# Performance work log

Measured on AMD Instinct MI355X. Metric: run time of the kernel, lower is better.

Reference implementation:

```python
import jax, jax.numpy as jnp
import numpy as np


def setup_inputs() -> dict:
    key = jax.random.key(0)
    ks = jax.random.split(key, 4)
    B, S, D, U = 4, 4096, 128, 64
    x = jax.random.normal(ks[0], (B, S, D), dtype=jnp.float32)
    Wq = jax.random.normal(ks[1], (D, U), dtype=jnp.float32) * (1.0 / np.sqrt(D))
    Wk = jax.random.normal(ks[2], (D, U), dtype=jnp.float32) * (1.0 / np.sqrt(D))
    Wv = jax.random.normal(ks[3], (D, U), dtype=jnp.float32) * (1.0 / np.sqrt(D))
    bq = jnp.zeros((U,), dtype=jnp.float32)
    bk = jnp.zeros((U,), dtype=jnp.float32)
    bv = jnp.zeros((U,), dtype=jnp.float32)
    return {"x": x, "Wq": Wq, "bq": bq, "Wk": Wk, "bk": bk, "Wv": Wv, "bv": bv}


def reference(x, Wq, bq, Wk, bk, Wv, bv):
    # Single-head, unscaled, unmasked attention (faithful to the Keras layer).
    q = jnp.einsum("bsd,du->bsu", x, Wq) + bq  # [B,S,U]
    k = jnp.einsum("bsd,du->bsu", x, Wk) + bk  # [B,S,U]
    v = jnp.einsum("bsd,du->bsu", x, Wv) + bv  # [B,S,U]
    scores = jnp.einsum("bsu,btu->bst", q, k)  # [B,S,S], no 1/sqrt(d) scaling
    attn = jax.nn.softmax(scores, axis=-1)
    return jnp.einsum("bst,btu->bsu", attn, v)  # [B,S,U]
```

## Files before the change

### kernel.cpp

```cpp
#include <hip/hip_runtime.h>
#include <hip/hip_fp16.h>
#include <math.h>

#define SEQ   4096
#define DIM   128
#define UDIM  64
#define BATCH 4
#define BS    (BATCH*SEQ)
#define NT    (SEQ/64)
#define NSPLIT 6

typedef _Float16 h8 __attribute__((ext_vector_type(8)));
typedef _Float16 h4 __attribute__((ext_vector_type(4)));
typedef _Float16 h2 __attribute__((ext_vector_type(2)));
typedef float    f4 __attribute__((ext_vector_type(4)));

#define MFMA_K32(a,b,c) __builtin_amdgcn_mfma_f32_16x16x32_f16((a),(b),(c),0,0,0)

__device__ __forceinline__ h2 pk2(float a, float b) {
  return __builtin_bit_cast(h2, __builtin_amdgcn_cvt_pkrtz(a, b));
}
__device__ __forceinline__ float fexp2(float x) {
#if __has_builtin(__builtin_amdgcn_exp2f)
  return __builtin_amdgcn_exp2f(x);
#else
  return exp2f(x);
#endif
}

#define WT_STRIDE 272
#define KB_STRIDE 144
#define L2E 1.44269504088896f


__global__ __launch_bounds__(256, 2) void proj_mfma(
    const float* __restrict__ x,
    const float* __restrict__ Wq, const float* __restrict__ bq,
    const float* __restrict__ Wk, const float* __restrict__ bk,
    const float* __restrict__ Wv, const float* __restrict__ bv,
    _Float16* __restrict__ qf, _Float16* __restrict__ kswz, _Float16* __restrict__ vswz)
{
  const int tid  = threadIdx.x;
  const int lane = tid & 63, wv = tid >> 6;
  const int n = lane & 15, quad = lane >> 4;
  const int r0 = blockIdx.x * 64;

  __shared__ __align__(16) char wlds[3][UDIM * WT_STRIDE];
  __shared__ __align__(16) char kbnc[4 * 16 * KB_STRIDE];

  #pragma unroll
  for (int p = 0; p < 3; ++p) {
    const float* __restrict__ W = (p == 0) ? Wq : ((p == 1) ? Wk : Wv);
    #pragma unroll
    for (int i = 0; i < 8; ++i) {
      const int idx = i*256 + tid;
      const int nn  = idx & 63;
      const int k4  = (idx >> 6) * 4;
      const float w0 = W[(k4+0)*UDIM + nn];
      const float w1 = W[(k4+1)*UDIM + nn];
      const float w2 = W[(k4+2)*UDIM + nn];
      const float w3 = W[(k4+3)*UDIM + nn];
      int2 wd;
      wd.x = __builtin_bit_cast(int, pk2(w0, w1));
      wd.y = __builtin_bit_cast(int, pk2(w2, w3));
      *(int2*)(wlds[p] + nn*WT_STRIDE + k4*2) = wd;
    }
  }

  const int row = r0 + wv*16 + n;
  h8 xa[4];
  #pragma unroll
  for (int ks = 0; ks < 4; ++ks) {
    const float* xp = x + (size_t)row*DIM + ks*32 + quad*8;
    const f4 a = *(const f4*)xp, b = *(const f4*)(xp + 4);
    int4 pkd;
    pkd.x = __builtin_bit_cast(int, pk2(a[0], a[1]));
    pkd.y = __builtin_bit_cast(int, pk2(a[2], a[3]));
    pkd.z = __builtin_bit_cast(int, pk2(b[0], b[1]));
    pkd.w = __builtin_bit_cast(int, pk2(b[2], b[3]));
    xa[ks] = __builtin_bit_cast(h8, pkd);
  }
  __syncthreads();

  const int b  = r0 / SEQ;
  const int kb = ((r0 % SEQ) >> 4) + wv;
  const int vt = (r0 % SEQ) >> 6;

  #pragma unroll
  for (int p = 0; p < 3; ++p) {
    const float* __restrict__ bias = (p == 0) ? bq : ((p == 1) ? bk : bv);
    f4 acc[4];
    #pragma unroll
    for (int nt = 0; nt < 4; ++nt) acc[nt] = (f4){0.f,0.f,0.f,0.f};
    #pragma unroll
    for (int ks = 0; ks < 4; ++ks)
      #pragma unroll
      for (int nt = 0; nt < 4; ++nt) {
        const h8 wf = *(const h8*)(wlds[p] + (nt*16 + n)*WT_STRIDE + (ks*32 + quad*8)*2);
        acc[nt] = MFMA_K32(xa[ks], wf, acc[nt]);
      }
    #pragma unroll
    for (int nt = 0; nt < 4; ++nt) {
      const float bb = bias[nt*16 + n];
      #pragma unroll
      for (int r = 0; r < 4; ++r) acc[nt][r] += bb;
    }

    if (p == 0) {
      #pragma unroll
      for (int nt = 0; nt < 4; ++nt)
        #pragma unroll
        for (int r = 0; r < 4; ++r) acc[nt][r] *= L2E;
      const int par = lane & 1;
      const unsigned sel = par ? 0x03020706u : 0x05040100u;
      #pragma unroll
      for (int nt = 0; nt < 4; ++nt)
        #pragma unroll
        for (int pp = 0; pp < 2; ++pp) {
          const int r = 2*pp;
          unsigned A  = __builtin_bit_cast(unsigned, pk2(acc[nt][r], acc[nt][r+1]));
          unsigned Bs = (unsigned)__builtin_amdgcn_mov_dpp((int)A, 0xB1, 0xF, 0xF, true);
          unsigned w  = __builtin_amdgcn_perm(Bs, A, sel);
          const int orow = r0 + wv*16 + 4*quad + r + par;
          const int ocol = nt*16 + n - par;
          *(unsigned*)((char*)qf + ((size_t)orow*UDIM + ocol)*2) = w;
        }
    } else if (p == 1) {
      char* base = kbnc + wv*(16*KB_STRIDE);
      #pragma unroll
      for (int nt = 0; nt < 4; ++nt)
        #pragma unroll
        for (int r = 0; r < 4; ++r)
          *(_Float16*)(base + (4*quad + r)*KB_STRIDE + (nt*16 + n)*2) =
              (_Float16)acc[nt][r];
      _Float16* kdst = kswz + (size_t)b*SEQ*UDIM;
      #pragma unroll
      for (int ks = 0; ks < 2; ++ks) {
        const h8 f = *(const h8*)(base + n*KB_STRIDE + ks*64 + quad*16);
        *(h8*)(kdst + ((size_t)(kb*2 + ks)*64 + lane)*8) = f;
      }
    } else {
      _Float16* vdst = vswz + (size_t)b*SEQ*UDIM + (size_t)vt*4096;
      const int hh = wv >> 1;
      const int qp = 2*(wv & 1) + (quad >> 1);
      const int jb = (quad & 1) * 4;
      #pragma unroll
      for (int nt = 0; nt < 4; ++nt) {
        int2 t;
        t.x = __builtin_bit_cast(int, pk2(acc[nt][0], acc[nt][1]));
        t.y = __builtin_bit_cast(int, pk2(acc[nt][2], acc[nt][3]));
        *(int2*)(vdst + (hh*4 + nt)*512 + (16*qp + n)*8 + jb) = t;
      }
    }
  }
}

__global__ __launch_bounds__(256, 3) void flash_attn_t(
    const _Float16* __restrict__ qf, const _Float16* __restrict__ kswz,
    const _Float16* __restrict__ vswz,
    _Float16* __restrict__ opart, float* __restrict__ Mp, float* __restrict__ Lp)
{
  const int qt = blockIdx.x, b = blockIdx.y, sp = blockIdx.z;
  const int ns = gridDim.z;
  const int kt0 = (sp * NT) / ns;
  const int kt1 = ((sp + 1) * NT) / ns;
  const int tid = threadIdx.x;
  const int lane = tid & 63, wid = tid >> 6;
  const int n = lane & 15, quad = lane >> 4;
  const int qbase = qt*128 + wid*32;

  const _Float16* __restrict__ qb = qf + (size_t)b*SEQ*UDIM;
  const _Float16* kpl = kswz + (size_t)b*SEQ*UDIM + (size_t)kt0*4096 + lane*8;
  const _Float16* kph = kpl + 2048;
  const _Float16* vpl = vswz + (size_t)b*SEQ*UDIM + (size_t)kt0*4096 + lane*8;
  const _Float16* vph = vpl + 2048;

  h8 qB[2][2];
  #pragma unroll
  for (int nt = 0; nt < 2; ++nt)
    #pragma unroll
    for (int ks = 0; ks < 2; ++ks)
      qB[nt][ks] = *(const h8*)(qb + (size_t)(qbase + nt*16 + n)*UDIM + ks*32 + quad*8);

  f4 O[4][2], Ol[2];
  #pragma unroll
  for (int ut = 0; ut < 4; ++ut)
    #pragma unroll
    for (int nt = 0; nt < 2; ++nt) O[ut][nt] = (f4){0.f,0.f,0.f,0.f};
  Ol[0] = (f4){0.f,0.f,0.f,0.f};
  Ol[1] = (f4){0.f,0.f,0.f,0.f};

  float M[2] = {-1e30f, -1e30f};

  h8 ones8;
  { const _Float16 o = (_Float16)1.0f;
    #pragma unroll
    for (int i = 0; i < 8; ++i) ones8[i] = o; }

  const int alo4 = ((32*((lane >> 4) & 1) + (lane & 15)) << 2);
  const int ahi4 = alo4 + 64;
  const bool qlo = (lane < 32);

  h8 ka[4][2];
  ka[0][0] = *(const h8*)(kpl);        ka[0][1] = *(const h8*)(kpl +  512);
  ka[1][0] = *(const h8*)(kpl + 1024); ka[1][1] = *(const h8*)(kpl + 1536);
  ka[2][0] = *(const h8*)(kph);        ka[2][1] = *(const h8*)(kph +  512);
  ka[3][0] = *(const h8*)(kph + 1024); ka[3][1] = *(const h8*)(kph + 1536);

  for (int t = kt0; t < kt1; ++t) {
    h8 va0[4];
    va0[0] = *(const h8*)(vpl);        va0[1] = *(const h8*)(vpl +  512);
    va0[2] = *(const h8*)(vpl + 1024); va0[3] = *(const h8*)(vpl + 1536);

    f4 S[4][2];
    #pragma unroll
    for (int mt = 0; mt < 4; ++mt)
      #pragma unroll
      for (int nt = 0; nt < 2; ++nt) S[mt][nt] = (f4){0.f,0.f,0.f,0.f};
    #pragma unroll
    for (int ks = 0; ks < 2; ++ks)
      #pragma unroll
      for (int mt = 0; mt < 4; ++mt)
        #pragma unroll
        for (int nt = 0; nt < 2; ++nt)
          S[mt][nt] = MFMA_K32(ka[mt][ks], qB[nt][ks], S[mt][nt]);

    if (t + 1 < kt1) {
      kpl += 4096; kph += 4096;
      ka[0][0] = *(const h8*)(kpl);        ka[0][1] = *(const h8*)(kpl +  512);
      ka[1][0] = *(const h8*)(kpl + 1024); ka[1][1] = *(const h8*)(kpl + 1536);
      ka[2][0] = *(const h8*)(kph);        ka[2][1] = *(const h8*)(kph +  512);
      ka[3][0] = *(const h8*)(kph + 1024); ka[3][1] = *(const h8*)(kph + 1536);
    }

    float mn[2];
    #pragma unroll
    for (int nt = 0; nt < 2; ++nt) {
      float m0 = fmaxf(fmaxf(S[0][nt][0], S[0][nt][1]), fmaxf(S[0][nt][2], S[0][nt][3]));
      float m1 = fmaxf(fmaxf(S[1][nt][0], S[1][nt][1]), fmaxf(S[1][nt][2], S[1][nt][3]));
      float m2 = fmaxf(fmaxf(S[2][nt][0], S[2][nt][1]), fmaxf(S[2][nt][2], S[2][nt][3]));
      float m3 = fmaxf(fmaxf(S[3][nt][0], S[3][nt][1]), fmaxf(S[3][nt][2], S[3][nt][3]));
      float rm = fmaxf(fmaxf(m0, m1), fmaxf(m2, m3));
      rm = fmaxf(rm, __shfl_xor(rm, 16));
      rm = fmaxf(rm, __shfl_xor(rm, 32));
      mn[nt] = fmaxf(M[nt], rm);
    }

    const bool nochange = (mn[0] == M[0]) && (mn[1] == M[1]);
    if (!__all(nochange)) {
      #pragma unroll
      for (int nt = 0; nt < 2; ++nt) {
        const float alpha = fexp2(M[nt] - mn[nt]);
        #pragma unroll
        for (int ut = 0; ut < 4; ++ut)
          #pragma unroll
          for (int r = 0; r < 4; ++r) O[ut][nt][r] *= alpha;
        #pragma unroll
        for (int r = 0; r < 4; ++r) Ol[nt][r] *= alpha;
      }
    }
    M[0] = mn[0]; M[1] = mn[1];

    h4 pB[4][2];
    #pragma unroll
    for (int mt = 0; mt < 4; ++mt)
      #pragma unroll
      for (int nt = 0; nt < 2; ++nt) {
        #pragma unroll
        for (int r = 0; r < 4; ++r)
          S[mt][nt][r] = fexp2(S[mt][nt][r] - mn[nt]);
        int2 tt;
        tt.x = __builtin_bit_cast(int, pk2(S[mt][nt][0], S[mt][nt][1]));
        tt.y = __builtin_bit_cast(int, pk2(S[mt][nt][2], S[mt][nt][3]));
        pB[mt][nt] = __builtin_bit_cast(h4, tt);
      }

    h8 pb32a[2];
    #pragma unroll
    for (int nt = 0; nt < 2; ++nt) {
      const int2 X = __builtin_bit_cast(int2, pB[0][nt]);
      const int2 Y = __builtin_bit_cast(int2, pB[1][nt]);
      int4 o;
      { int a0 = __builtin_amdgcn_ds_bpermute(alo4, X.x);
        int b0 = __builtin_amdgcn_ds_bpermute(alo4, Y.x);
        int a1 = __builtin_amdgcn_ds_bpermute(alo4, X.y);
        int b1 = __builtin_amdgcn_ds_bpermute(alo4, Y.y);
        int a2 = __builtin_amdgcn_ds_bpermute(ahi4, X.x);
        int b2 = __builtin_amdgcn_ds_bpermute(ahi4, Y.x);
        int a3 = __builtin_amdgcn_ds_bpermute(ahi4, X.y);
        int b3 = __builtin_amdgcn_ds_bpermute(ahi4, Y.y);
        o.x = qlo ? a0 : b0; o.y = qlo ? a1 : b1;
        o.z = qlo ? a2 : b2; o.w = qlo ? a3 : b3; }
      pb32a[nt] = __builtin_bit_cast(h8, o);
    }

    h8 va1[4];
    va1[0] = *(const h8*)(vph);        va1[1] = *(const h8*)(vph +  512);
    va1[2] = *(const h8*)(vph + 1024); va1[3] = *(const h8*)(vph + 1536);

    #pragma unroll
    for (int ut = 0; ut < 4; ++ut)
      #pragma unroll
      for (int nt = 0; nt < 2; ++nt)
        O[ut][nt] = MFMA_K32(va0[ut], pb32a[nt], O[ut][nt]);
    #pragma unroll
    for (int nt = 0; nt < 2; ++nt)
      Ol[nt] = MFMA_K32(ones8, pb32a[nt], Ol[nt]);

    h8 pb32b[2];
    #pragma unroll
    for (int nt = 0; nt < 2; ++nt) {
      const int2 X = __builtin_bit_cast(int2, pB[2][nt]);
      const int2 Y = __builtin_bit_cast(int2, pB[3][nt]);
      int4 o;
      { int a0 = __builtin_amdgcn_ds_bpermute(alo4, X.x);
        int b0 = __builtin_amdgcn_ds_bpermute(alo4, Y.x);
        int a1 = __builtin_amdgcn_ds_bpermute(alo4, X.y);
        int b1 = __builtin_amdgcn_ds_bpermute(alo4, Y.y);
        int a2 = __builtin_amdgcn_ds_bpermute(ahi4, X.x);
        int b2 = __builtin_amdgcn_ds_bpermute(ahi4, Y.x);
        int a3 = __builtin_amdgcn_ds_bpermute(ahi4, X.y);
        int b3 = __builtin_amdgcn_ds_bpermute(ahi4, Y.y);
        o.x = qlo ? a0 : b0; o.y = qlo ? a1 : b1;
        o.z = qlo ? a2 : b2; o.w = qlo ? a3 : b3; }
      pb32b[nt] = __builtin_bit_cast(h8, o);
    }

    #pragma unroll
    for (int ut = 0; ut < 4; ++ut)
      #pragma unroll
      for (int nt = 0; nt < 2; ++nt)
        O[ut][nt] = MFMA_K32(va1[ut], pb32b[nt], O[ut][nt]);
    #pragma unroll
    for (int nt = 0; nt < 2; ++nt)
      Ol[nt] = MFMA_K32(ones8, pb32b[nt], Ol[nt]);

    vpl += 4096; vph += 4096;
  }

  const size_t rowg = (size_t)sp*BS + (size_t)b*SEQ + qbase;
  #pragma unroll
  for (int nt = 0; nt < 2; ++nt) {
    char* __restrict__ orow = (char*)(opart + (rowg + nt*16 + n)*UDIM);
    #pragma unroll
    for (int ut = 0; ut < 4; ++ut)
      #pragma unroll
      for (int p = 0; p < 2; ++p)
        *(unsigned*)(orow + (ut*16 + quad*4 + 2*p)*2) =
            __builtin_bit_cast(unsigned, pk2(O[ut][nt][2*p], O[ut][nt][2*p+1]));
    if (quad == 0) {
      Mp[rowg + nt*16 + n] = M[nt];
      Lp[rowg + nt*16 + n] = Ol[nt][0];
    }
  }
}

__global__ __launch_bounds__(256) void merge_out(
    const _Float16* __restrict__ opart, const float* __restrict__ Mp,
    const float* __restrict__ Lp, float* __restrict__ out, int nsplit)
{
  const int tid = threadIdx.x;
  const int row = blockIdx.x*16 + (tid >> 4);
  const int u4  = (tid & 15) * 4;
  float M = -1e30f;
  for (int s = 0; s < nsplit; ++s) M = fmaxf(M, Mp[(size_t)s*BS + row]);
  f4 num = (f4){0.f,0.f,0.f,0.f};
  float den = 0.f;
  for (int s = 0; s < nsplit; ++s) {
    const float w = fexp2(Mp[(size_t)s*BS + row] - M);
    den += w * Lp[(size_t)s*BS + row];
    const h4 op = *(const h4*)(opart + ((size_t)s*BS + row)*UDIM + u4);
    #pragma unroll
    for (int i = 0; i < 4; ++i) num[i] += w * (float)op[i];
  }
  const float dinv = 1.f / den;
  *(f4*)(out + (size_t)row*UDIM + u4) = num * dinv;
}

extern "C" void kernel_launch(void* const* d_in, const int* in_sizes, int n_in,
                              void* d_out, int out_size, void* d_ws, size_t ws_size,
                              hipStream_t stream) {
  (void)in_sizes; (void)n_in; (void)out_size;
  const float* x  = (const float*)d_in[0];
  const float* Wq = (const float*)d_in[1];
  const float* bq = (const float*)d_in[2];
  const float* Wk = (const float*)d_in[3];
  const float* bk = (const float*)d_in[4];
  const float* Wv = (const float*)d_in[5];
  const float* bv = (const float*)d_in[6];
  float* out = (float*)d_out;

  char* ws = (char*)d_ws;
  const size_t fBytes = (size_t)BS * UDIM * 2;
  auto need = [](int nsp) {
    return (size_t)3*BS*UDIM*2 + (size_t)nsp*BS*4*2 + (size_t)nsp*BS*UDIM*2;
  };
  int nsplit;
  if      (ws_size >= need(NSPLIT)) nsplit = NSPLIT;
  else if (ws_size >= need(4))      nsplit = 4;
  else if (ws_size >= need(2))      nsplit = 2;
  else                              nsplit = 1;

  _Float16* qf   = (_Float16*)(ws);
  _Float16* kswz = (_Float16*)(ws + fBytes);
  _Float16* vswz = (_Float16*)(ws + 2*fBytes);
  float* Mp      = (float*)(ws + 3*fBytes);
  float* Lp      = (float*)(ws + 3*fBytes + (size_t)nsplit*BS*4);
  _Float16* opart = (_Float16*)(ws + 3*fBytes + (size_t)nsplit*BS*8);

  proj_mfma<<<dim3(BS/64), 256, 0, stream>>>(x, Wq, bq, Wk, bk, Wv, bv, qf, kswz, vswz);
  flash_attn_t<<<dim3(SEQ/128, BATCH, nsplit), 256, 0, stream>>>(
      qf, kswz, vswz, opart, Mp, Lp);
  merge_out<<<dim3(BS/16), 256, 0, stream>>>(opart, Mp, Lp, out, nsplit);
}
```

Before: 109.6 us.

## Stage K/V tiles into double-buffered LDS via global_load_lds shared across waves

Replaces per-wave direct global loads of K and V tiles with a block-wide asynchronous global-to-LDS copy into a double buffer. Each wave stages one quarter of the next tile, then all waves read K and V fragments from LDS. Before, each of the four waves fetched the full tile from global/L2 itself, so this cuts that redundant traffic and overlaps the fetch with compute. In exchange it adds 32KB of LDS per block, which may limit occupancy, plus a barrier per iteration and LDS read latency. It also relies on the barrier to ensure the async copies have completed.

```diff
diff --git a/kernel.cpp b/kernel.cpp
--- a/kernel.cpp
+++ b/kernel.cpp
@@ -26,6 +26,12 @@
 #else
   return exp2f(x);
 #endif
+}
+
+__device__ __forceinline__ void stage16(const void* g, void* l) {
+  __builtin_amdgcn_global_load_lds(
+      (const __attribute__((address_space(1))) unsigned int*)g,
+      (__attribute__((address_space(3))) unsigned int*)l, 16, 0, 0);
 }
 
 #define WT_STRIDE 272
@@ -169,12 +175,24 @@
   const int n = lane & 15, quad = lane >> 4;
   const int qbase = qt*128 + wid*32;
 
+  __shared__ __align__(16) char kv[2][16384];
+
+  const char* __restrict__ kbase = (const char*)kswz + (size_t)b*SEQ*UDIM*2;
+  const char* __restrict__ vbase = (const char*)vswz + (size_t)b*SEQ*UDIM*2;
+  const int s0 = wid*2;
+  const int lb = lane*16;
+
+  {
+    const char* kb_ = kbase + (size_t)kt0*8192;
+    const char* vb_ = vbase + (size_t)kt0*8192;
+    #pragma unroll
+    for (int s = 0; s < 2; ++s) {
+      stage16(kb_ + (s0+s)*1024 + lb, &kv[0][(s0+s)*1024]);
+      stage16(vb_ + (s0+s)*1024 + lb, &kv[0][8192 + (s0+s)*1024]);
+    }
+  }
+
   const _Float16* __restrict__ qb = qf + (size_t)b*SEQ*UDIM;
-  const _Float16* kpl = kswz + (size_t)b*SEQ*UDIM + (size_t)kt0*4096 + lane*8;
-  const _Float16* kph = kpl + 2048;
-  const _Float16* vpl = vswz + (size_t)b*SEQ*UDIM + (size_t)kt0*4096 + lane*8;
-  const _Float16* vph = vpl + 2048;
-
   h8 qB[2][2];
   #pragma unroll
   for (int nt = 0; nt < 2; ++nt)
@@ -201,16 +219,30 @@
   const int ahi4 = alo4 + 64;
   const bool qlo = (lane < 32);
 
-  h8 ka[4][2];
-  ka[0][0] = *(const h8*)(kpl);        ka[0][1] = *(const h8*)(kpl +  512);
-  ka[1][0] = *(const h8*)(kpl + 1024); ka[1][1] = *(const h8*)(kpl + 1536);
-  ka[2][0] = *(const h8*)(kph);        ka[2][1] = *(const h8*)(kph +  512);
-  ka[3][0] = *(const h8*)(kph + 1024); ka[3][1] = *(const h8*)(kph + 1536);
-
+  __syncthreads();
+
+  int cur = 0;
   for (int t = kt0; t < kt1; ++t) {
-    h8 va0[4];
-    va0[0] = *(const h8*)(vpl);        va0[1] = *(const h8*)(vpl +  512);
-    va0[2] = *(const h8*)(vpl + 1024); va0[3] = *(const h8*)(vpl + 1536);
+    if (t + 1 < kt1) {
+      const char* kb_ = kbase + (size_t)(t+1)*8192;
+      const char* vb_ = vbase + (size_t)(t+1)*8192;
+      char* dst = kv[cur ^ 1];
+      #pragma unroll
+      for (int s = 0; s < 2; ++s) {
+        stage16(kb_ + (s0+s)*1024 + lb, dst + (s0+s)*1024);
+        stage16(vb_ + (s0+s)*1024 + lb, dst + 8192 + (s0+s)*1024);
+      }
+    }
+
+    const char* Kl = kv[cur] + lb;
+    const char* Vl = Kl + 8192;
+
+    h8 ka[4][2];
+    #pragma unroll
+    for (int mt = 0; mt < 4; ++mt)
+      #pragma unroll
+      for (int ks = 0; ks < 2; ++ks)
+        ka[mt][ks] = *(const h8*)(Kl + (mt*2 + ks)*1024);
 
     f4 S[4][2];
     #pragma unroll
@@ -224,14 +256,6 @@
         #pragma unroll
         for (int nt = 0; nt < 2; ++nt)
           S[mt][nt] = MFMA_K32(ka[mt][ks], qB[nt][ks], S[mt][nt]);
-
-    if (t + 1 < kt1) {
-      kpl += 4096; kph += 4096;
-      ka[0][0] = *(const h8*)(kpl);        ka[0][1] = *(const h8*)(kpl +  512);
-      ka[1][0] = *(const h8*)(kpl + 1024); ka[1][1] = *(const h8*)(kpl + 1536);
-      ka[2][0] = *(const h8*)(kph);        ka[2][1] = *(const h8*)(kph +  512);
-      ka[3][0] = *(const h8*)(kph + 1024); ka[3][1] = *(const h8*)(kph + 1536);
-    }
 
     float mn[2];
     #pragma unroll
@@ -294,9 +318,9 @@
       pb32a[nt] = __builtin_bit_cast(h8, o);
     }
 
-    h8 va1[4];
-    va1[0] = *(const h8*)(vph);        va1[1] = *(const h8*)(vph +  512);
-    va1[2] = *(const h8*)(vph + 1024); va1[3] = *(const h8*)(vph + 1536);
+    h8 va0[4];
+    #pragma unroll
+    for (int ut = 0; ut < 4; ++ut) va0[ut] = *(const h8*)(Vl + ut*1024);
 
     #pragma unroll
     for (int ut = 0; ut < 4; ++ut)
@@ -326,6 +350,10 @@
       pb32b[nt] = __builtin_bit_cast(h8, o);
     }
 
+    h8 va1[4];
+    #pragma unroll
+    for (int ut = 0; ut < 4; ++ut) va1[ut] = *(const h8*)(Vl + (4 + ut)*1024);
+
     #pragma unroll
     for (int ut = 0; ut < 4; ++ut)
       #pragma unroll
@@ -335,7 +363,8 @@
     for (int nt = 0; nt < 2; ++nt)
       Ol[nt] = MFMA_K32(ones8, pb32b[nt], Ol[nt]);
 
-    vpl += 4096; vph += 4096;
+    if (t + 1 < kt1) __syncthreads();
+    cur ^= 1;
   }
 
   const size_t rowg = (size_t)sp*BS + (size_t)b*SEQ + qbase;
```

Result: slower. 114.0 us (+4.0%).

## Fuse projection, attention and merge into one cooperative kernel with grid syncs

Applied to the files above, without the earlier changes.

Merges the three launches (QKV projection, split-K flash attention, merge) into a single cooperative kernel of 256 blocks × 512 threads, separated by grid-wide syncs. The split count drops from 6 to 4 so that the 256 blocks × 8 waves map exactly onto the attention work items. This removes launch overhead and inter-kernel gaps. In exchange it adds grid barriers and gives less parallelism in the attention phase, with 2048 waves on 256 CUs. The workspace-size fallback is removed.

```diff
diff --git a/kernel.cpp b/kernel.cpp
--- a/kernel.cpp
+++ b/kernel.cpp
@@ -1,6 +1,9 @@
 #include <hip/hip_runtime.h>
 #include <hip/hip_fp16.h>
+#include <hip/hip_cooperative_groups.h>
 #include <math.h>
+
+namespace cg = cooperative_groups;
 
 #define SEQ   4096
 #define DIM   128
@@ -8,7 +11,7 @@
 #define BATCH 4
 #define BS    (BATCH*SEQ)
 #define NT    (SEQ/64)
-#define NSPLIT 6
+#define NSPLIT 4
 
 typedef _Float16 h8 __attribute__((ext_vector_type(8)));
 typedef _Float16 h4 __attribute__((ext_vector_type(4)));
@@ -33,116 +36,131 @@
 #define L2E 1.44269504088896f
 
 
-__global__ __launch_bounds__(256, 2) void proj_mfma(
+__global__ __launch_bounds__(512, 2) void fused_attn(
     const float* __restrict__ x,
     const float* __restrict__ Wq, const float* __restrict__ bq,
     const float* __restrict__ Wk, const float* __restrict__ bk,
     const float* __restrict__ Wv, const float* __restrict__ bv,
-    _Float16* __restrict__ qf, _Float16* __restrict__ kswz, _Float16* __restrict__ vswz)
+    _Float16* __restrict__ qf, _Float16* __restrict__ kswz,
+    _Float16* __restrict__ vswz,
+    _Float16* __restrict__ opart, float* __restrict__ Mp,
+    float* __restrict__ Lp, float* __restrict__ out)
 {
+  cg::grid_group grid = cg::this_grid();
   const int tid  = threadIdx.x;
-  const int lane = tid & 63, wv = tid >> 6;
+  const int lane = tid & 63, wid = tid >> 6;
   const int n = lane & 15, quad = lane >> 4;
-  const int r0 = blockIdx.x * 64;
 
   __shared__ __align__(16) char wlds[3][UDIM * WT_STRIDE];
   __shared__ __align__(16) char kbnc[4 * 16 * KB_STRIDE];
 
-  #pragma unroll
-  for (int p = 0; p < 3; ++p) {
-    const float* __restrict__ W = (p == 0) ? Wq : ((p == 1) ? Wk : Wv);
-    #pragma unroll
-    for (int i = 0; i < 8; ++i) {
-      const int idx = i*256 + tid;
-      const int nn  = idx & 63;
-      const int k4  = (idx >> 6) * 4;
-      const float w0 = W[(k4+0)*UDIM + nn];
-      const float w1 = W[(k4+1)*UDIM + nn];
-      const float w2 = W[(k4+2)*UDIM + nn];
-      const float w3 = W[(k4+3)*UDIM + nn];
-      int2 wd;
-      wd.x = __builtin_bit_cast(int, pk2(w0, w1));
-      wd.y = __builtin_bit_cast(int, pk2(w2, w3));
-      *(int2*)(wlds[p] + nn*WT_STRIDE + k4*2) = wd;
-    }
-  }
-
-  const int row = r0 + wv*16 + n;
-  h8 xa[4];
-  #pragma unroll
-  for (int ks = 0; ks < 4; ++ks) {
-    const float* xp = x + (size_t)row*DIM + ks*32 + quad*8;
-    const f4 a = *(const f4*)xp, b = *(const f4*)(xp + 4);
-    int4 pkd;
-    pkd.x = __builtin_bit_cast(int, pk2(a[0], a[1]));
-    pkd.y = __builtin_bit_cast(int, pk2(a[2], a[3]));
-    pkd.z = __builtin_bit_cast(int, pk2(b[0], b[1]));
-    pkd.w = __builtin_bit_cast(int, pk2(b[2], b[3]));
-    xa[ks] = __builtin_bit_cast(h8, pkd);
-  }
-  __syncthreads();
-
-  const int b  = r0 / SEQ;
-  const int kb = ((r0 % SEQ) >> 4) + wv;
-  const int vt = (r0 % SEQ) >> 6;
-
-  #pragma unroll
-  for (int p = 0; p < 3; ++p) {
-    const float* __restrict__ bias = (p == 0) ? bq : ((p == 1) ? bk : bv);
-    f4 acc[4];
-    #pragma unroll
-    for (int nt = 0; nt < 4; ++nt) acc[nt] = (f4){0.f,0.f,0.f,0.f};
-    #pragma unroll
-    for (int ks = 0; ks < 4; ++ks)
+  {
+    const int r0 = blockIdx.x * 64;
+
+    #pragma unroll
+    for (int p = 0; p < 3; ++p) {
+      const float* __restrict__ W = (p == 0) ? Wq : ((p == 1) ? Wk : Wv);
+      #pragma unroll
+      for (int i = 0; i < 4; ++i) {
+        const int idx = i*512 + tid;
+        const int nn  = idx & 63;
+        const int k4  = (idx >> 6) * 4;
+        const float w0 = W[(k4+0)*UDIM + nn];
+        const float w1 = W[(k4+1)*UDIM + nn];
+        const float w2 = W[(k4+2)*UDIM + nn];
+        const float w3 = W[(k4+3)*UDIM + nn];
+        int2 wd;
+        wd.x = __builtin_bit_cast(int, pk2(w0, w1));
+        wd.y = __builtin_bit_cast(int, pk2(w2, w3));
+        *(int2*)(wlds[p] + nn*WT_STRIDE + k4*2) = wd;
+      }
+    }
+
+    const int g    = wid & 3;
+    const int half = wid >> 2;
+    const int row  = r0 + g*16 + n;
+    h8 xa[4];
+    #pragma unroll
+    for (int ks = 0; ks < 4; ++ks) {
+      const float* xp = x + (size_t)row*DIM + ks*32 + quad*8;
+      const f4 a = *(const f4*)xp, bb2 = *(const f4*)(xp + 4);
+      int4 pkd;
+      pkd.x = __builtin_bit_cast(int, pk2(a[0], a[1]));
+      pkd.y = __builtin_bit_cast(int, pk2(a[2], a[3]));
+      pkd.z = __builtin_bit_cast(int, pk2(bb2[0], bb2[1]));
+      pkd.w = __builtin_bit_cast(int, pk2(bb2[2], bb2[3]));
+      xa[ks] = __builtin_bit_cast(h8, pkd);
+    }
+    __syncthreads();
+
+    const int b  = r0 / SEQ;
+    const int kb = ((r0 % SEQ) >> 4) + g;
+    const int vt = (r0 % SEQ) >> 6;
+
+    auto gemm16 = [&](const char* wp, const float* bias, f4* acc) {
+      #pragma unroll
+      for (int nt = 0; nt < 4; ++nt) acc[nt] = (f4){0.f,0.f,0.f,0.f};
+      #pragma unroll
+      for (int ks = 0; ks < 4; ++ks)
+        #pragma unroll
+        for (int nt = 0; nt < 4; ++nt) {
+          const h8 wf = *(const h8*)(wp + (nt*16 + n)*WT_STRIDE + (ks*32 + quad*8)*2);
+          acc[nt] = MFMA_K32(xa[ks], wf, acc[nt]);
+        }
       #pragma unroll
       for (int nt = 0; nt < 4; ++nt) {
-        const h8 wf = *(const h8*)(wlds[p] + (nt*16 + n)*WT_STRIDE + (ks*32 + quad*8)*2);
-        acc[nt] = MFMA_K32(xa[ks], wf, acc[nt]);
-      }
-    #pragma unroll
-    for (int nt = 0; nt < 4; ++nt) {
-      const float bb = bias[nt*16 + n];
-      #pragma unroll
-      for (int r = 0; r < 4; ++r) acc[nt][r] += bb;
-    }
-
-    if (p == 0) {
-      #pragma unroll
-      for (int nt = 0; nt < 4; ++nt)
-        #pragma unroll
-        for (int r = 0; r < 4; ++r) acc[nt][r] *= L2E;
-      const int par = lane & 1;
-      const unsigned sel = par ? 0x03020706u : 0x05040100u;
-      #pragma unroll
-      for (int nt = 0; nt < 4; ++nt)
-        #pragma unroll
-        for (int pp = 0; pp < 2; ++pp) {
-          const int r = 2*pp;
-          unsigned A  = __builtin_bit_cast(unsigned, pk2(acc[nt][r], acc[nt][r+1]));
-          unsigned Bs = (unsigned)__builtin_amdgcn_mov_dpp((int)A, 0xB1, 0xF, 0xF, true);
-          unsigned w  = __builtin_amdgcn_perm(Bs, A, sel);
-          const int orow = r0 + wv*16 + 4*quad + r + par;
-          const int ocol = nt*16 + n - par;
-          *(unsigned*)((char*)qf + ((size_t)orow*UDIM + ocol)*2) = w;
+        const float bb = bias[nt*16 + n];
+        #pragma unroll
+        for (int r = 0; r < 4; ++r) acc[nt][r] += bb;
+      }
+    };
+
+    if (half == 0) {
+      {
+        f4 acc[4];
+        gemm16(wlds[0], bq, acc);
+        #pragma unroll
+        for (int nt = 0; nt < 4; ++nt)
+          #pragma unroll
+          for (int r = 0; r < 4; ++r) acc[nt][r] *= L2E;
+        const int par = lane & 1;
+        const unsigned sel = par ? 0x03020706u : 0x05040100u;
+        #pragma unroll
+        for (int nt = 0; nt < 4; ++nt)
+          #pragma unroll
+          for (int pp = 0; pp < 2; ++pp) {
+            const int r = 2*pp;
+            unsigned A  = __builtin_bit_cast(unsigned, pk2(acc[nt][r], acc[nt][r+1]));
+            unsigned Bs = (unsigned)__builtin_amdgcn_mov_dpp((int)A, 0xB1, 0xF, 0xF, true);
+            unsigned w  = __builtin_amdgcn_perm(Bs, A, sel);
+            const int orow = r0 + g*16 + 4*quad + r + par;
+            const int ocol = nt*16 + n - par;
+            *(unsigned*)((char*)qf + ((size_t)orow*UDIM + ocol)*2) = w;
+          }
+      }
+      {
+        f4 acc[4];
+        gemm16(wlds[1], bk, acc);
+        char* base = kbnc + g*(16*KB_STRIDE);
+        #pragma unroll
+        for (int nt = 0; nt < 4; ++nt)
+          #pragma unroll
+          for (int r = 0; r < 4; ++r)
+            *(_Float16*)(base + (4*quad + r)*KB_STRIDE + (nt*16 + n)*2) =
+                (_Float16)acc[nt][r];
+        _Float16* kdst = kswz + (size_t)b*SEQ*UDIM;
+        #pragma unroll
+        for (int ks = 0; ks < 2; ++ks) {
+          const h8 f = *(const h8*)(base + n*KB_STRIDE + ks*64 + quad*16);
+          *(h8*)(kdst + ((size_t)(kb*2 + ks)*64 + lane)*8) = f;
         }
-    } else if (p == 1) {
-      char* base = kbnc + wv*(16*KB_STRIDE);
-      #pragma unroll
-      for (int nt = 0; nt < 4; ++nt)
-        #pragma unroll
-        for (int r = 0; r < 4; ++r)
-          *(_Float16*)(base + (4*quad + r)*KB_STRIDE + (nt*16 + n)*2) =
-              (_Float16)acc[nt][r];
-      _Float16* kdst = kswz + (size_t)b*SEQ*UDIM;
-      #pragma unroll
-      for (int ks = 0; ks < 2; ++ks) {
-        const h8 f = *(const h8*)(base + n*KB_STRIDE + ks*64 + quad*16);
-        *(h8*)(kdst + ((size_t)(kb*2 + ks)*64 + lane)*8) = f;
       }
     } else {
+      f4 acc[4];
+      gemm16(wlds[2], bv, acc);
       _Float16* vdst = vswz + (size_t)b*SEQ*UDIM + (size_t)vt*4096;
-      const int hh = wv >> 1;
-      const int qp = 2*(wv & 1) + (quad >> 1);
+      const int hh = g >> 1;
+      const int qp = 2*(g & 1) + (quad >> 1);
       const int jb = (quad & 1) * 4;
       #pragma unroll
       for (int nt = 0; nt < 4; ++nt) {
@@ -153,234 +171,238 @@
       }
     }
   }
-}
-
-__global__ __launch_bounds__(256, 3) void flash_attn_t(
-    const _Float16* __restrict__ qf, const _Float16* __restrict__ kswz,
-    const _Float16* __restrict__ vswz,
-    _Float16* __restrict__ opart, float* __restrict__ Mp, float* __restrict__ Lp)
-{
-  const int qt = blockIdx.x, b = blockIdx.y, sp = blockIdx.z;
-  const int ns = gridDim.z;
-  const int kt0 = (sp * NT) / ns;
-  const int kt1 = ((sp + 1) * NT) / ns;
-  const int tid = threadIdx.x;
-  const int lane = tid & 63, wid = tid >> 6;
-  const int n = lane & 15, quad = lane >> 4;
-  const int qbase = qt*128 + wid*32;
-
-  const _Float16* __restrict__ qb = qf + (size_t)b*SEQ*UDIM;
-  const _Float16* kpl = kswz + (size_t)b*SEQ*UDIM + (size_t)kt0*4096 + lane*8;
-  const _Float16* kph = kpl + 2048;
-  const _Float16* vpl = vswz + (size_t)b*SEQ*UDIM + (size_t)kt0*4096 + lane*8;
-  const _Float16* vph = vpl + 2048;
-
-  h8 qB[2][2];
-  #pragma unroll
-  for (int nt = 0; nt < 2; ++nt)
-    #pragma unroll
-    for (int ks = 0; ks < 2; ++ks)
-      qB[nt][ks] = *(const h8*)(qb + (size_t)(qbase + nt*16 + n)*UDIM + ks*32 + quad*8);
-
-  f4 O[4][2], Ol[2];
-  #pragma unroll
-  for (int ut = 0; ut < 4; ++ut)
-    #pragma unroll
-    for (int nt = 0; nt < 2; ++nt) O[ut][nt] = (f4){0.f,0.f,0.f,0.f};
-  Ol[0] = (f4){0.f,0.f,0.f,0.f};
-  Ol[1] = (f4){0.f,0.f,0.f,0.f};
-
-  float M[2] = {-1e30f, -1e30f};
-
-  h8 ones8;
-  { const _Float16 o = (_Float16)1.0f;
-    #pragma unroll
-    for (int i = 0; i < 8; ++i) ones8[i] = o; }
-
-  const int alo4 = ((32*((lane >> 4) & 1) + (lane & 15)) << 2);
-  const int ahi4 = alo4 + 64;
-  const bool qlo = (lane < 32);
-
-  h8 ka[4][2];
-  ka[0][0] = *(const h8*)(kpl);        ka[0][1] = *(const h8*)(kpl +  512);
-  ka[1][0] = *(const h8*)(kpl + 1024); ka[1][1] = *(const h8*)(kpl + 1536);
-  ka[2][0] = *(const h8*)(kph);        ka[2][1] = *(const h8*)(kph +  512);
-  ka[3][0] = *(const h8*)(kph + 1024); ka[3][1] = *(const h8*)(kph + 1536);
-
-  for (int t = kt0; t < kt1; ++t) {
-    h8 va0[4];
-    va0[0] = *(const h8*)(vpl);        va0[1] = *(const h8*)(vpl +  512);
-    va0[2] = *(const h8*)(vpl + 1024); va0[3] = *(const h8*)(vpl + 1536);
-
-    f4 S[4][2];
-    #pragma unroll
-    for (int mt = 0; mt < 4; ++mt)
-      #pragma unroll
-      for (int nt = 0; nt < 2; ++nt) S[mt][nt] = (f4){0.f,0.f,0.f,0.f};
-    #pragma unroll
-    for (int ks = 0; ks < 2; ++ks)
+
+  __threadfence();
+  grid.sync();
+
+  {
+    const int Wg  = blockIdx.x*8 + wid;
+    const int o   = Wg >> 2;
+    const int qt  = o & 31;
+    const int fb  = (o >> 5) & 3;
+    const int sp  = o >> 7;
+    const int kt0 = sp * (NT/NSPLIT);
+    const int kt1 = kt0 + (NT/NSPLIT);
+    const int qbase = qt*128 + (Wg & 3)*32;
+
+    const _Float16* __restrict__ qb = qf + (size_t)fb*SEQ*UDIM;
+    const _Float16* kpl = kswz + (size_t)fb*SEQ*UDIM + (size_t)kt0*4096 + lane*8;
+    const _Float16* kph = kpl + 2048;
+    const _Float16* vpl = vswz + (size_t)fb*SEQ*UDIM + (size_t)kt0*4096 + lane*8;
+    const _Float16* vph = vpl + 2048;
+
+    h8 qB[2][2];
+    #pragma unroll
+    for (int nt = 0; nt < 2; ++nt)
+      #pragma unroll
+      for (int ks = 0; ks < 2; ++ks)
+        qB[nt][ks] = *(const h8*)(qb + (size_t)(qbase + nt*16 + n)*UDIM + ks*32 + quad*8);
+
+    f4 O[4][2], Ol[2];
+    #pragma unroll
+    for (int ut = 0; ut < 4; ++ut)
+      #pragma unroll
+      for (int nt = 0; nt < 2; ++nt) O[ut][nt] = (f4){0.f,0.f,0.f,0.f};
+    Ol[0] = (f4){0.f,0.f,0.f,0.f};
+    Ol[1] = (f4){0.f,0.f,0.f,0.f};
+
+    float M[2] = {-1e30f, -1e30f};
+
+    h8 ones8;
+    { const _Float16 one = (_Float16)1.0f;
+      #pragma unroll
+      for (int i = 0; i < 8; ++i) ones8[i] = one; }
+
+    const int alo4 = ((32*((lane >> 4) & 1) + (lane & 15)) << 2);
+    const int ahi4 = alo4 + 64;
+    const bool qlo = (lane < 32);
+
+    h8 ka[4][2];
+    ka[0][0] = *(const h8*)(kpl);        ka[0][1] = *(const h8*)(kpl +  512);
+    ka[1][0] = *(const h8*)(kpl + 1024); ka[1][1] = *(const h8*)(kpl + 1536);
+    ka[2][0] = *(const h8*)(kph);        ka[2][1] = *(const h8*)(kph +  512);
+    ka[3][0] = *(const h8*)(kph + 1024); ka[3][1] = *(const h8*)(kph + 1536);
+
+    for (int t = kt0; t < kt1; ++t) {
+      h8 va0[4];
+      va0[0] = *(const h8*)(vpl);        va0[1] = *(const h8*)(vpl +  512);
+      va0[2] = *(const h8*)(vpl + 1024); va0[3] = *(const h8*)(vpl + 1536);
+
+      f4 S[4][2];
       #pragma unroll
       for (int mt = 0; mt < 4; ++mt)
         #pragma unroll
+        for (int nt = 0; nt < 2; ++nt) S[mt][nt] = (f4){0.f,0.f,0.f,0.f};
+      #pragma unroll
+      for (int ks = 0; ks < 2; ++ks)
+        #pragma unroll
+        for (int mt = 0; mt < 4; ++mt)
+          #pragma unroll
+          for (int nt = 0; nt < 2; ++nt)
+            S[mt][nt] = MFMA_K32(ka[mt][ks], qB[nt][ks], S[mt][nt]);
+
+      if (t + 1 < kt1) {
+        kpl += 4096; kph += 4096;
+        ka[0][0] = *(const h8*)(kpl);        ka[0][1] = *(const h8*)(kpl +  512);
+        ka[1][0] = *(const h8*)(kpl + 1024); ka[1][1] = *(const h8*)(kpl + 1536);
+        ka[2][0] = *(const h8*)(kph);        ka[2][1] = *(const h8*)(kph +  512);
+        ka[3][0] = *(const h8*)(kph + 1024); ka[3][1] = *(const h8*)(kph + 1536);
+      }
+
+      float mn[2];
+      #pragma unroll
+      for (int nt = 0; nt < 2; ++nt) {
+        float m0 = fmaxf(fmaxf(S[0][nt][0], S[0][nt][1]), fmaxf(S[0][nt][2], S[0][nt][3]));
+        float m1 = fmaxf(fmaxf(S[1][nt][0], S[1][nt][1]), fmaxf(S[1][nt][2], S[1][nt][3]));
+        float m2 = fmaxf(fmaxf(S[2][nt][0], S[2][nt][1]), fmaxf(S[2][nt][2], S[2][nt][3]));
+        float m3 = fmaxf(fmaxf(S[3][nt][0], S[3][nt][1]), fmaxf(S[3][nt][2], S[3][nt][3]));
+        float rm = fmaxf(fmaxf(m0, m1), fmaxf(m2, m3));
+        rm = fmaxf(rm, __shfl_xor(rm, 16));
+        rm = fmaxf(rm, __shfl_xor(rm, 32));
+        mn[nt] = fmaxf(M[nt], rm);
+      }
+
+      const bool nochange = (mn[0] == M[0]) && (mn[1] == M[1]);
+      if (!__all(nochange)) {
+        #pragma unroll
+        for (int nt = 0; nt < 2; ++nt) {
+          const float alpha = fexp2(M[nt] - mn[nt]);
+          #pragma unroll
+          for (int ut = 0; ut < 4; ++ut)
+            #pragma unroll
+            for (int r = 0; r < 4; ++r) O[ut][nt][r] *= alpha;
+          #pragma unroll
+          for (int r = 0; r < 4; ++r) Ol[nt][r] *= alpha;
+        }
+      }
+      M[0] = mn[0]; M[1] = mn[1];
+
+      h4 pB[4][2];
+      #pragma unroll
+      for (int mt = 0; mt < 4; ++mt)
+        #pragma unroll
+        for (int nt = 0; nt < 2; ++nt) {
+          #pragma unroll
+          for (int r = 0; r < 4; ++r)
+            S[mt][nt][r] = fexp2(S[mt][nt][r] - mn[nt]);
+          int2 tt;
+          tt.x = __builtin_bit_cast(int, pk2(S[mt][nt][0], S[mt][nt][1]));
+          tt.y = __builtin_bit_cast(int, pk2(S[mt][nt][2], S[mt][nt][3]));
+          pB[mt][nt] = __builtin_bit_cast(h4, tt);
+        }
+
+      h8 pb32a[2];
+      #pragma unroll
+      for (int nt = 0; nt < 2; ++nt) {
+        const int2 X = __builtin_bit_cast(int2, pB[0][nt]);
+        const int2 Y = __builtin_bit_cast(int2, pB[1][nt]);
+        int4 oo;
+        { int a0 = __builtin_amdgcn_ds_bpermute(alo4, X.x);
+          int b0 = __builtin_amdgcn_ds_bpermute(alo4, Y.x);
+          int a1 = __builtin_amdgcn_ds_bpermute(alo4, X.y);
+          int b1 = __builtin_amdgcn_ds_bpermute(alo4, Y.y);
+          int a2 = __builtin_amdgcn_ds_bpermute(ahi4, X.x);
+          int b2 = __builtin_amdgcn_ds_bpermute(ahi4, Y.x);
+          int a3 = __builtin_amdgcn_ds_bpermute(ahi4, X.y);
+          int b3 = __builtin_amdgcn_ds_bpermute(ahi4, Y.y);
+          oo.x = qlo ? a0 : b0; oo.y = qlo ? a1 : b1;
+          oo.z = qlo ? a2 : b2; oo.w = qlo ? a3 : b3; }
+        pb32a[nt] = __builtin_bit_cast(h8, oo);
+      }
+
+      h8 va1[4];
+      va1[0] = *(const h8*)(vph);        va1[1] = *(const h8*)(vph +  512);
+      va1[2] = *(const h8*)(vph + 1024); va1[3] = *(const h8*)(vph + 1536);
+
+      #pragma unroll
+      for (int ut = 0; ut < 4; ++ut)
+        #pragma unroll
         for (int nt = 0; nt < 2; ++nt)
-          S[mt][nt] = MFMA_K32(ka[mt][ks], qB[nt][ks], S[mt][nt]);
-
-    if (t + 1 < kt1) {
-      kpl += 4096; kph += 4096;
-      ka[0][0] = *(const h8*)(kpl);        ka[0][1] = *(const h8*)(kpl +  512);
-      ka[1][0] = *(const h8*)(kpl + 1024); ka[1][1] = *(const h8*)(kpl + 1536);
-      ka[2][0] = *(const h8*)(kph);        ka[2][1] = *(const h8*)(kph +  512);
-      ka[3][0] = *(const h8*)(kph + 1024); ka[3][1] = *(const h8*)(kph + 1536);
-    }
-
-    float mn[2];
+          O[ut][nt] = MFMA_K32(va0[ut], pb32a[nt], O[ut][nt]);
+      #pragma unroll
+      for (int nt = 0; nt < 2; ++nt)
+        Ol[nt] = MFMA_K32(ones8, pb32a[nt], Ol[nt]);
+
+      h8 pb32b[2];
+      #pragma unroll
+      for (int nt = 0; nt < 2; ++nt) {
+        const int2 X = __builtin_bit_cast(int2, pB[2][nt]);
+        const int2 Y = __builtin_bit_cast(int2, pB[3][nt]);
+        int4 oo;
+        { int a0 = __builtin_amdgcn_ds_bpermute(alo4, X.x);
+          int b0 = __builtin_amdgcn_ds_bpermute(alo4, Y.x);
+          int a1 = __builtin_amdgcn_ds_bpermute(alo4, X.y);
+          int b1 = __builtin_amdgcn_ds_bpermute(alo4, Y.y);
+          int a2 = __builtin_amdgcn_ds_bpermute(ahi4, X.x);
+          int b2 = __builtin_amdgcn_ds_bpermute(ahi4, Y.x);
+          int a3 = __builtin_amdgcn_ds_bpermute(ahi4, X.y);
+          int b3 = __builtin_amdgcn_ds_bpermute(ahi4, Y.y);
+          oo.x = qlo ? a0 : b0; oo.y = qlo ? a1 : b1;
+          oo.z = qlo ? a2 : b2; oo.w = qlo ? a3 : b3; }
+        pb32b[nt] = __builtin_bit_cast(h8, oo);
+      }
+
+      #pragma unroll
+      for (int ut = 0; ut < 4; ++ut)
+        #pragma unroll
+        for (int nt = 0; nt < 2; ++nt)
+          O[ut][nt] = MFMA_K32(va1[ut], pb32b[nt], O[ut][nt]);
+      #pragma unroll
+      for (int nt = 0; nt < 2; ++nt)
+        Ol[nt] = MFMA_K32(ones8, pb32b[nt], Ol[nt]);
+
+      vpl += 4096; vph += 4096;
+    }
+
+    const size_t rowg = (size_t)sp*BS + (size_t)fb*SEQ + qbase;
     #pragma unroll
     for (int nt = 0; nt < 2; ++nt) {
-      float m0 = fmaxf(fmaxf(S[0][nt][0], S[0][nt][1]), fmaxf(S[0][nt][2], S[0][nt][3]));
-      float m1 = fmaxf(fmaxf(S[1][nt][0], S[1][nt][1]), fmaxf(S[1][nt][2], S[1][nt][3]));
-      float m2 = fmaxf(fmaxf(S[2][nt][0], S[2][nt][1]), fmaxf(S[2][nt][2], S[2][nt][3]));
-      float m3 = fmaxf(fmaxf(S[3][nt][0], S[3][nt][1]), fmaxf(S[3][nt][2], S[3][nt][3]));
-      float rm = fmaxf(fmaxf(m0, m1), fmaxf(m2, m3));
-      rm = fmaxf(rm, __shfl_xor(rm, 16));
-      rm = fmaxf(rm, __shfl_xor(rm, 32));
-      mn[nt] = fmaxf(M[nt], rm);
-    }
-
-    const bool nochange = (mn[0] == M[0]) && (mn[1] == M[1]);
-    if (!__all(nochange)) {
-      #pragma unroll
-      for (int nt = 0; nt < 2; ++nt) {
-        const float alpha = fexp2(M[nt] - mn[nt]);
-        #pragma unroll
-        for (int ut = 0; ut < 4; ++ut)
-          #pragma unroll
-          for (int r = 0; r < 4; ++r) O[ut][nt][r] *= alpha;
-        #pragma unroll
-        for (int r = 0; r < 4; ++r) Ol[nt][r] *= alpha;
-      }
-    }
-    M[0] = mn[0]; M[1] = mn[1];
-
-    h4 pB[4][2];
-    #pragma unroll
-    for (int mt = 0; mt < 4; ++mt)
-      #pragma unroll
-      for (int nt = 0; nt < 2; ++nt) {
-        #pragma unroll
-        for (int r = 0; r < 4; ++r)
-          S[mt][nt][r] = fexp2(S[mt][nt][r] - mn[nt]);
-        int2 tt;
-        tt.x = __builtin_bit_cast(int, pk2(S[mt][nt][0], S[mt][nt][1]));
-        tt.y = __builtin_bit_cast(int, pk2(S[mt][nt][2], S[mt][nt][3]));
-        pB[mt][nt] = __builtin_bit_cast(h4, tt);
-      }
-
-    h8 pb32a[2];
-    #pragma unroll
-    for (int nt = 0; nt < 2; ++nt) {
-      const int2 X = __builtin_bit_cast(int2, pB[0][nt]);
-      const int2 Y = __builtin_bit_cast(int2, pB[1][nt]);
-      int4 o;
-      { int a0 = __builtin_amdgcn_ds_bpermute(alo4, X.x);
-        int b0 = __builtin_amdgcn_ds_bpermute(alo4, Y.x);
-        int a1 = __builtin_amdgcn_ds_bpermute(alo4, X.y);
-        int b1 = __builtin_amdgcn_ds_bpermute(alo4, Y.y);
-        int a2 = __builtin_amdgcn_ds_bpermute(ahi4, X.x);
-        int b2 = __builtin_amdgcn_ds_bpermute(ahi4, Y.x);
-        int a3 = __builtin_amdgcn_ds_bpermute(ahi4, X.y);
-        int b3 = __builtin_amdgcn_ds_bpermute(ahi4, Y.y);
-        o.x = qlo ? a0 : b0; o.y = qlo ? a1 : b1;
-        o.z = qlo ? a2 : b2; o.w = qlo ? a3 : b3; }
-      pb32a[nt] = __builtin_bit_cast(h8, o);
-    }
-
-    h8 va1[4];
-    va1[0] = *(const h8*)(vph);        va1[1] = *(const h8*)(vph +  512);
-    va1[2] = *(const h8*)(vph + 1024); va1[3] = *(const h8*)(vph + 1536);
-
-    #pragma unroll
-    for (int ut = 0; ut < 4; ++ut)
-      #pragma unroll
-      for (int nt = 0; nt < 2; ++nt)
-        O[ut][nt] = MFMA_K32(va0[ut], pb32a[nt], O[ut][nt]);
-    #pragma unroll
-    for (int nt = 0; nt < 2; ++nt)
-      Ol[nt] = MFMA_K32(ones8, pb32a[nt], Ol[nt]);
-
-    h8 pb32b[2];
-    #pragma unroll
-    for (int nt = 0; nt < 2; ++nt) {
-      const int2 X = __builtin_bit_cast(int2, pB[2][nt]);
-      const int2 Y = __builtin_bit_cast(int2, pB[3][nt]);
-      int4 o;
-      { int a0 = __builtin_amdgcn_ds_bpermute(alo4, X.x);
-        int b0 = __builtin_amdgcn_ds_bpermute(alo4, Y.x);
-        int a1 = __builtin_amdgcn_ds_bpermute(alo4, X.y);
-        int b1 = __builtin_amdgcn_ds_bpermute(alo4, Y.y);
-        int a2 = __builtin_amdgcn_ds_bpermute(ahi4, X.x);
-        int b2 = __builtin_amdgcn_ds_bpermute(ahi4, Y.x);
-        int a3 = __builtin_amdgcn_ds_bpermute(ahi4, X.y);
-        int b3 = __builtin_amdgcn_ds_bpermute(ahi4, Y.y);
-        o.x = qlo ? a0 : b0; o.y = qlo ? a1 : b1;
-        o.z = qlo ? a2 : b2; o.w = qlo ? a3 : b3; }
-      pb32b[nt] = __builtin_bit_cast(h8, o);
-    }
-
-    #pragma unroll
-    for (int ut = 0; ut < 4; ++ut)
-      #pragma unroll
-      for (int nt = 0; nt < 2; ++nt)
-        O[ut][nt] = MFMA_K32(va1[ut], pb32b[nt], O[ut][nt]);
-    #pragma unroll
-    for (int nt = 0; nt < 2; ++nt)
-      Ol[nt] = MFMA_K32(ones8, pb32b[nt], Ol[nt]);
-
-    vpl += 4096; vph += 4096;
+      char* __restrict__ orow = (char*)(opart + (rowg + nt*16 + n)*UDIM);
+      #pragma unroll
+      for (int ut = 0; ut < 4; ++ut)
+        #pragma unroll
+        for (int p = 0; p < 2; ++p)
+          *(unsigned*)(orow + (ut*16 + quad*4 + 2*p)*2) =
+              __builtin_bit_cast(unsigned, pk2(O[ut][nt][2*p], O[ut][nt][2*p+1]));
+      if (quad == 0) {
+        Mp[rowg + nt*16 + n] = M[nt];
+        Lp[rowg + nt*16 + n] = Ol[nt][0];
+      }
+    }
   }
 
-  const size_t rowg = (size_t)sp*BS + (size_t)b*SEQ + qbase;
-  #pragma unroll
-  for (int nt = 0; nt < 2; ++nt) {
-    char* __restrict__ orow = (char*)(opart + (rowg + nt*16 + n)*UDIM);
-    #pragma unroll
-    for (int ut = 0; ut < 4; ++ut)
-      #pragma unroll
-      for (int p = 0; p < 2; ++p)
-        *(unsigned*)(orow + (ut*16 + quad*4 + 2*p)*2) =
-            __builtin_bit_cast(unsigned, pk2(O[ut][nt][2*p], O[ut][nt][2*p+1]));
-    if (quad == 0) {
-      Mp[rowg + nt*16 + n] = M[nt];
-      Lp[rowg + nt*16 + n] = Ol[nt][0];
+  __threadfence();
+  grid.sync();
+
+  {
+    #pragma unroll
+    for (int it = 0; it < 2; ++it) {
+      const int task = it*(256*512) + blockIdx.x*512 + tid;
+      const int row  = task >> 4;
+      const int u4   = (task & 15) * 4;
+      float Mm = -1e30f;
+      #pragma unroll
+      for (int s = 0; s < NSPLIT; ++s) Mm = fmaxf(Mm, Mp[(size_t)s*BS + row]);
+      f4 num = (f4){0.f,0.f,0.f,0.f};
+      float den = 0.f;
+      #pragma unroll
+      for (int s = 0; s < NSPLIT; ++s) {
+        const float w = fexp2(Mp[(size_t)s*BS + row] - Mm);
+        den += w * Lp[(size_t)s*BS + row];
+        const h4 op = *(const h4*)(opart + ((size_t)s*BS + row)*UDIM + u4);
+        #pragma unroll
+        for (int i = 0; i < 4; ++i) num[i] += w * (float)op[i];
+      }
+      const float dinv = 1.f / den;
+      *(f4*)(out + (size_t)row*UDIM + u4) = num * dinv;
     }
   }
-}
-
-__global__ __launch_bounds__(256) void merge_out(
-    const _Float16* __restrict__ opart, const float* __restrict__ Mp,
-    const float* __restrict__ Lp, float* __restrict__ out, int nsplit)
-{
-  const int tid = threadIdx.x;
-  const int row = blockIdx.x*16 + (tid >> 4);
-  const int u4  = (tid & 15) * 4;
-  float M = -1e30f;
-  for (int s = 0; s < nsplit; ++s) M = fmaxf(M, Mp[(size_t)s*BS + row]);
-  f4 num = (f4){0.f,0.f,0.f,0.f};
-  float den = 0.f;
-  for (int s = 0; s < nsplit; ++s) {
-    const float w = fexp2(Mp[(size_t)s*BS + row] - M);
-    den += w * Lp[(size_t)s*BS + row];
-    const h4 op = *(const h4*)(opart + ((size_t)s*BS + row)*UDIM + u4);
-    #pragma unroll
-    for (int i = 0; i < 4; ++i) num[i] += w * (float)op[i];
-  }
-  const float dinv = 1.f / den;
-  *(f4*)(out + (size_t)row*UDIM + u4) = num * dinv;
 }
 
 extern "C" void kernel_launch(void* const* d_in, const int* in_sizes, int n_in,
                               void* d_out, int out_size, void* d_ws, size_t ws_size,
                               hipStream_t stream) {
-  (void)in_sizes; (void)n_in; (void)out_size;
+  (void)in_sizes; (void)n_in; (void)out_size; (void)ws_size;
   const float* x  = (const float*)d_in[0];
   const float* Wq = (const float*)d_in[1];
   const float* bq = (const float*)d_in[2];
@@ -392,24 +414,19 @@
 
   char* ws = (char*)d_ws;
   const size_t fBytes = (size_t)BS * UDIM * 2;
-  auto need = [](int nsp) {
-    return (size_t)3*BS*UDIM*2 + (size_t)nsp*BS*4*2 + (size_t)nsp*BS*UDIM*2;
+
+  _Float16* qf    = (_Float16*)(ws);
+  _Float16* kswz  = (_Float16*)(ws + fBytes);
+  _Float16* vswz  = (_Float16*)(ws + 2*fBytes);
+  float*    Mp    = (float*)(ws + 3*fBytes);
+  float*    Lp    = (float*)(ws + 3*fBytes + (size_t)NSPLIT*BS*4);
+  _Float16* opart = (_Float16*)(ws + 3*fBytes + (size_t)NSPLIT*BS*8);
+
+  void* kargs[] = {
+    (void*)&x, (void*)&Wq, (void*)&bq, (void*)&Wk, (void*)&bk,
+    (void*)&Wv, (void*)&bv, (void*)&qf, (void*)&kswz, (void*)&vswz,
+    (void*)&opart, (void*)&Mp, (void*)&Lp, (void*)&out
   };
-  int nsplit;
-  if      (ws_size >= need(NSPLIT)) nsplit = NSPLIT;
-  else if (ws_size >= need(4))      nsplit = 4;
-  else if (ws_size >= need(2))      nsplit = 2;
-  else                              nsplit = 1;
-
-  _Float16* qf   = (_Float16*)(ws);
-  _Float16* kswz = (_Float16*)(ws + fBytes);
-  _Float16* vswz = (_Float16*)(ws + 2*fBytes);
-  float* Mp      = (float*)(ws + 3*fBytes);
-  float* Lp      = (float*)(ws + 3*fBytes + (size_t)nsplit*BS*4);
-  _Float16* opart = (_Float16*)(ws + 3*fBytes + (size_t)nsplit*BS*8);
-
-  proj_mfma<<<dim3(BS/64), 256, 0, stream>>>(x, Wq, bq, Wk, bk, Wv, bv, qf, kswz, vswz);
-  flash_attn_t<<<dim3(SEQ/128, BATCH, nsplit), 256, 0, stream>>>(
-      qf, kswz, vswz, opart, Mp, Lp);
-  merge_out<<<dim3(BS/16), 256, 0, stream>>>(opart, Mp, Lp, out, nsplit);
+  hipLaunchCooperativeKernel((const void*)fused_attn, dim3(256), dim3(512),
+                             kargs, 0, stream);
 }
```

New measurement: 294.9 us. +169.1%, slower.
